# Optimization experiments

Hardware: AMD Instinct MI355X
Metric: run time of the kernel (lower is better)

## Reference

```python
import jax, jax.numpy as jnp
import numpy as np

B, S, D = 4, 2048, 1024
H, HD = 16, 64
DFF = 4096
EPS = 1e-6


def setup_inputs() -> dict:
    key = jax.random.key(0)
    ks = jax.random.split(key, 16)
    sc = 0.02
    def w(k, shape):
        return jax.random.normal(k, shape, dtype=jnp.float32) * sc
    return {
        'x': jax.random.normal(ks[0], (B, S, D), dtype=jnp.float32),
        'wq': w(ks[1], (D, D)), 'bq': jnp.zeros((D,), jnp.float32),
        'wk': w(ks[2], (D, D)), 'bk': jnp.zeros((D,), jnp.float32),
        'wv': w(ks[3], (D, D)), 'bv': jnp.zeros((D,), jnp.float32),
        'wo': w(ks[4], (D, D)), 'bo': jnp.zeros((D,), jnp.float32),
        'w1': w(ks[5], (D, DFF)), 'b1': jnp.zeros((DFF,), jnp.float32),
        'w2': w(ks[6], (DFF, D)), 'b2': jnp.zeros((D,), jnp.float32),
        'ln1_a': jnp.ones((D,), jnp.float32), 'ln1_b': jnp.zeros((D,), jnp.float32),
        'ln2_a': jnp.ones((D,), jnp.float32), 'ln2_b': jnp.zeros((D,), jnp.float32),
    }


def layernorm(x, alpha, bias):
    # Matches torch module: std is unbiased (ddof=1), divide by (std + eps)
    mean = jnp.mean(x, axis=-1, keepdims=True)
    var = jnp.sum((x - mean) ** 2, axis=-1, keepdims=True) / (x.shape[-1] - 1)
    std = jnp.sqrt(var)
    return alpha * ((x - mean) / (std + EPS)) + bias


def mha(x, wq, bq, wk, bk, wv, bv, wo, bo):
    q = (x @ wq + bq).reshape(B, S, H, HD)
    k = (x @ wk + bk).reshape(B, S, H, HD)
    v = (x @ wv + bv).reshape(B, S, H, HD)
    scores = jnp.einsum('bqhd,bkhd->bhqk', q, k) / jnp.sqrt(jnp.float32(HD))
    attn = jax.nn.softmax(scores, axis=-1)
    out = jnp.einsum('bhqk,bkhd->bqhd', attn, v).reshape(B, S, D)
    return out @ wo + bo


def reference(x, wq, bq, wk, bk, wv, bv, wo, bo, w1, b1, w2, b2,
              ln1_a, ln1_b, ln2_a, ln2_b):
    # Residual 1: x + MHA(LN(x))   (dropout = identity, eval mode)
    x = x + mha(layernorm(x, ln1_a, ln1_b), wq, bq, wk, bk, wv, bv, wo, bo)
    # Residual 2: x + FFN(LN(x))
    h = layernorm(x, ln2_a, ln2_b)
    ffn = jax.nn.relu(h @ w1 + b1) @ w2 + b2
    return x + ffn
```

## Files before the change

### kernel.cpp

```cpp
#include <hip/hip_runtime.h>

#define S_ 2048
#define D_ 1024

typedef unsigned short u16;
typedef unsigned int u32;
typedef __bf16 bf16x8 __attribute__((ext_vector_type(8)));
typedef unsigned short us8 __attribute__((ext_vector_type(8)));
typedef unsigned short us4 __attribute__((ext_vector_type(4)));
typedef unsigned int u32x4 __attribute__((ext_vector_type(4)));
typedef float f32x4 __attribute__((ext_vector_type(4)));

#if __has_builtin(__builtin_amdgcn_exp2f)
#define EXP2(x) __builtin_amdgcn_exp2f(x)
#else
#define EXP2(x) exp2f(x)
#endif

static __device__ __forceinline__ u16 f2bf(float f) {
  unsigned u = __builtin_bit_cast(unsigned, f);
  u += 0x7fffu + ((u >> 16) & 1u);
  return (u16)(u >> 16);
}

static __device__ __forceinline__ unsigned cvtpk_bf16(float lo, float hi) {
  unsigned r;
  asm("v_cvt_pk_bf16_f32 %0, %1, %2" : "=v"(r) : "v"(lo), "v"(hi));
  return r;
}

static __device__ __forceinline__ f32x4 mfma16(bf16x8 a, bf16x8 b, f32x4 c) {
  return __builtin_amdgcn_mfma_f32_16x16x32_bf16(a, b, c, 0, 0, 0);
}

static __device__ __forceinline__ void gload16(const void* g, void* lds) {
  __builtin_amdgcn_global_load_lds((const __attribute__((address_space(1))) void*)g,
                                   (__attribute__((address_space(3))) void*)lds, 16, 0, 0);
}

__global__ __launch_bounds__(256) void prep_kernel(
    const float* __restrict__ wq, const float* __restrict__ wk, const float* __restrict__ wv,
    const float* __restrict__ wo, const float* __restrict__ w1, const float* __restrict__ w2,
    const float* __restrict__ bq, const float* __restrict__ bk, const float* __restrict__ bv,
    u16* __restrict__ wqkv, u16* __restrict__ wot, u16* __restrict__ w1t,
    u16* __restrict__ w2t, float* __restrict__ bcat, float qs) {
  const int bid = blockIdx.x;
  const int tx = threadIdx.x, ty = threadIdx.y;
  if (bid >= 12288) {
    const int i = (bid - 12288) * 256 + ty * 32 + tx;
    bcat[i] = (i < 1024) ? bq[i] * qs : ((i < 2048) ? bk[i - 1024] : bv[i - 2048]);
    return;
  }
  const float* in;
  u16* out;
  int K, N, idx;
  float sc = 1.0f;
  if (bid < 4096) {
    K = 1024; N = 1024; idx = bid & 1023;
    if (bid < 1024)      { in = wq; out = wqkv;             sc = qs; }
    else if (bid < 2048) { in = wk; out = wqkv + (1 << 20); }
    else if (bid < 3072) { in = wv; out = wqkv + (2 << 20); }
    else                 { in = wo; out = wot; }
  } else if (bid < 8192) {
    in = w1; out = w1t; K = 1024; N = 4096; idx = bid - 4096;
  } else {
    in = w2; out = w2t; K = 4096; N = 1024; idx = bid - 8192;
  }
  const int nb = N >> 5;
  const int n0 = (idx % nb) * 32, k0 = (idx / nb) * 32;
  __shared__ float t[32][33];
#pragma unroll
  for (int i = 0; i < 4; i++)
    t[ty + 8 * i][tx] = in[(size_t)(k0 + ty + 8 * i) * N + n0 + tx];
  __syncthreads();
#pragma unroll
  for (int i = 0; i < 4; i++)
    out[(size_t)(n0 + ty + 8 * i) * K + k0 + tx] = f2bf(t[tx][ty + 8 * i] * sc);
}

__global__ __launch_bounds__(256) void ln_kernel(const float* __restrict__ in,
                                                 u16* __restrict__ out,
                                                 const float* __restrict__ alpha,
                                                 const float* __restrict__ beta) {
  const int row = blockIdx.x;
  const int tid = threadIdx.x;
  const float4 v = *(const float4*)(in + (size_t)row * D_ + tid * 4);
  float s = v.x + v.y + v.z + v.w;
  float ss = v.x * v.x + v.y * v.y + v.z * v.z + v.w * v.w;
#pragma unroll
  for (int off = 32; off >= 1; off >>= 1) {
    s += __shfl_xor(s, off);
    ss += __shfl_xor(ss, off);
  }
  __shared__ float red[8];
  const int w = tid >> 6, lane = tid & 63;
  if (lane == 0) { red[w] = s; red[4 + w] = ss; }
  __syncthreads();
  s = red[0] + red[1] + red[2] + red[3];
  ss = red[4] + red[5] + red[6] + red[7];
  const float mean = s * (1.0f / D_);
  const float var = (ss - s * mean) * (1.0f / (D_ - 1));
  const float inv = 1.0f / (sqrtf(var) + 1e-6f);
  const int j = tid * 4;
  const float4 av = *(const float4*)(alpha + j);
  const float4 bv = *(const float4*)(beta + j);
  us4 o;
  o[0] = f2bf((v.x - mean) * inv * av.x + bv.x);
  o[1] = f2bf((v.y - mean) * inv * av.y + bv.y);
  o[2] = f2bf((v.z - mean) * inv * av.z + bv.z);
  o[3] = f2bf((v.w - mean) * inv * av.w + bv.w);
  *(us4*)(out + (size_t)row * D_ + j) = o;
}

template <int OM, bool RELU, bool RESID>
__global__ __launch_bounds__(512, 2) void gemm_bt(const u16* __restrict__ A,
                                                  const u16* __restrict__ Bt,
                                                  const float* __restrict__ bias,
                                                  const float* __restrict__ resid,
                                                  void* __restrict__ outp,
                                                  void* __restrict__ out1,
                                                  void* __restrict__ out2, int N, int K) {
  __shared__ u16 lds[3 * 24576];
  const int tid = threadIdx.x;
  const int lane = tid & 63, w = tid >> 6;
  const int g = lane >> 4, r = lane & 15;
  const int wr = w >> 1, wc = w & 1;

  const int gx = gridDim.x;
  const int nwg = gx * gridDim.y;
  const int orig = blockIdx.y * gx + blockIdx.x;
  const int nid = (orig & 7) * (nwg >> 3) + (orig >> 3);
  const int bx = nid % gx, by = nid / gx;
  const size_t row0 = (size_t)by * 256;
  const int col0 = bx * 128;

  float bias4[4];
#pragma unroll
  for (int n = 0; n < 4; n++) bias4[n] = bias[col0 + wc * 64 + n * 16 + r];

  f32x4 acc[4][4];
#pragma unroll
  for (int m = 0; m < 4; m++)
#pragma unroll
    for (int n = 0; n < 4; n++) {
      f32x4 z = {bias4[n], bias4[n], bias4[n], bias4[n]};
      acc[m][n] = z;
    }

  const int lrow = w * 8 + (lane >> 3);
  const int scol = 8 * ((lane & 7) ^ (lane >> 3));
  const u16* gA = A + (row0 + lrow) * (size_t)K + scol;
  const u16* gB = Bt + ((size_t)col0 + lrow) * (size_t)K + scol;
  const int nt = K >> 6;
  const int sw = (r & 7) << 3;

  int bufi = 0;
#pragma unroll
  for (int t0 = 0; t0 < 2; t0++) {
    u16* dA = lds + t0 * 24576 + w * 512;
#pragma unroll
    for (int j = 0; j < 4; j++) gload16(gA + (size_t)(j * 64) * K + t0 * 64, dA + j * 4096);
#pragma unroll
    for (int j = 0; j < 2; j++)
      gload16(gB + (size_t)(j * 64) * K + t0 * 64, dA + 16384 + j * 4096);
  }

  for (int t = 0; t < nt; ++t) {
    if (t + 1 < nt)
      asm volatile("s_waitcnt vmcnt(6)" ::: "memory");
    else
      asm volatile("s_waitcnt vmcnt(0)" ::: "memory");
    __builtin_amdgcn_s_barrier();
    asm volatile("" ::: "memory");
    const bool st = (t + 2 < nt);
    const int bn = (bufi + 2 >= 3) ? bufi - 1 : bufi + 2;
    u16* dS = lds + bn * 24576 + w * 512;
    const size_t ko = (size_t)(t + 2) * 64;
    const u16* As_ = lds + bufi * 24576;
    const u16* Bs_ = As_ + 16384;
    bf16x8 bfr[2][4];

#pragma unroll
    for (int p = 0; p < 4; ++p) {
      bf16x8 a0 = __builtin_bit_cast(
          bf16x8, *(const us8*)(As_ + (wr * 64 + p * 16 + r) * 64 + ((g * 8) ^ sw)));
      bf16x8 a1 = __builtin_bit_cast(
          bf16x8, *(const us8*)(As_ + (wr * 64 + p * 16 + r) * 64 + ((32 + g * 8) ^ sw)));
      if (p == 0) {
#pragma unroll
        for (int kk = 0; kk < 2; kk++)
#pragma unroll
          for (int n = 0; n < 4; n++)
            bfr[kk][n] = __builtin_bit_cast(
                bf16x8,
                *(const us8*)(Bs_ + (wc * 64 + n * 16 + r) * 64 + ((kk * 32 + g * 8) ^ sw)));
      }
      if (st) {
        if (p == 0) {
          gload16(gA + ko, dS);
          gload16(gA + (size_t)64 * K + ko, dS + 4096);
        } else if (p == 1) {
          gload16(gA + (size_t)128 * K + ko, dS + 8192);
          gload16(gA + (size_t)192 * K + ko, dS + 12288);
        } else if (p == 2) {
          gload16(gB + ko, dS + 16384);
          gload16(gB + (size_t)64 * K + ko, dS + 20480);
        }
      }
      asm volatile("s_waitcnt lgkmcnt(0)" ::: "memory");
      __builtin_amdgcn_sched_barrier(0);
      __builtin_amdgcn_s_setprio(1);
#pragma unroll
      for (int n = 0; n < 4; n++) {
        acc[p][n] = mfma16(a0, bfr[0][n], acc[p][n]);
        acc[p][n] = mfma16(a1, bfr[1][n], acc[p][n]);
      }
      __builtin_amdgcn_s_setprio(0);
      if (p < 3) __builtin_amdgcn_s_barrier();
    }
    bufi = (bufi == 2) ? 0 : bufi + 1;
  }

#pragma unroll
  for (int m = 0; m < 4; m++)
#pragma unroll
    for (int n = 0; n < 4; n++) {
      if (OM == 2) {
        const int seg = col0 >> 10;
        const int cl = (col0 & 1023) + wc * 64 + n * 16 + r;
        if (seg == 2) {
          const int head = cl >> 6, hd = cl & 63;
          const size_t rg0 = row0 + wr * 64 + m * 16 + 4 * g;
          const int b = (int)(rg0 >> 11), s0 = (int)(rg0 & 2047);
          const int s0p = (s0 & ~63) | (s0 & 32) | ((s0 << 1) & 24) | ((s0 >> 2) & 4);
          us4 o;
#pragma unroll
          for (int i = 0; i < 4; i++) o[i] = f2bf(acc[m][n][i]);
          *(us4*)((u16*)out2 + (((size_t)(b * 16 + head) * 64 + hd) * S_ + s0p)) = o;
        } else {
          u16* dst = (u16*)(seg == 0 ? outp : out1);
#pragma unroll
          for (int i = 0; i < 4; i++) {
            const size_t rg = row0 + wr * 64 + m * 16 + 4 * g + i;
            dst[rg * D_ + cl] = f2bf(acc[m][n][i]);
          }
        }
      } else {
#pragma unroll
        for (int i = 0; i < 4; i++) {
          const size_t rg = row0 + wr * 64 + m * 16 + 4 * g + i;
          const int cg = col0 + wc * 64 + n * 16 + r;
          float v = acc[m][n][i];
          if (RESID) v += resid[rg * N + cg];
          if (RELU) v = fmaxf(v, 0.0f);
          if (OM == 1)
            ((float*)outp)[rg * N + cg] = v;
          else
            ((u16*)outp)[rg * N + cg] = f2bf(v);
        }
      }
    }
}

template <bool RELU>
__global__ __launch_bounds__(512, 2) void gemm_bt256(const u16* __restrict__ A,
                                                     const u16* __restrict__ Bt,
                                                     const float* __restrict__ bias,
                                                     u16* __restrict__ outp, int N, int K) {
  __shared__ u16 lds[2 * 32768];
  const int tid = threadIdx.x;
  const int lane = tid & 63, w = tid >> 6;
  const int g = lane >> 4, r = lane & 15;
  const int wr = w >> 2, wc = w & 3;
  const int gx = gridDim.x;
  const int nwg = gx * gridDim.y;
  const int orig = blockIdx.y * gx + blockIdx.x;
  const int nid = (orig & 7) * (nwg >> 3) + (orig >> 3);
  const int bx = nid % gx, by = nid / gx;
  const size_t row0 = (size_t)by * 256;
  const int col0 = bx * 256;

  float bias4[4];
#pragma unroll
  for (int n = 0; n < 4; n++) bias4[n] = bias[col0 + wc * 64 + n * 16 + r];

  f32x4 acc[8][4];
#pragma unroll
  for (int m = 0; m < 8; m++)
#pragma unroll
    for (int n = 0; n < 4; n++) {
      f32x4 z = {bias4[n], bias4[n], bias4[n], bias4[n]};
      acc[m][n] = z;
    }

  const int lrow = tid >> 3;
  const int scol = 8 * ((tid & 7) ^ (lrow & 7));
  const u16* gA = A + (row0 + lrow) * (size_t)K + scol;
  const u16* gB = Bt + ((size_t)col0 + lrow) * (size_t)K + scol;
  const int nt = K >> 6;
  const int sw = (r & 7) << 3;

  {
    u16* d = lds + w * 512;
#pragma unroll
    for (int j = 0; j < 4; j++) gload16(gA + (size_t)(j * 64) * K, d + j * 4096);
#pragma unroll
    for (int j = 0; j < 4; j++) gload16(gB + (size_t)(j * 64) * K, d + 16384 + j * 4096);
  }

  for (int t = 0; t < nt; ++t) {
    const u16* As_ = lds + (t & 1) * 32768;
    const u16* Bs_ = As_ + 16384;
    if (t + 1 < nt) {
      u16* d = lds + ((t + 1) & 1) * 32768 + w * 512;
      const size_t ko = (size_t)(t + 1) * 64;
#pragma unroll
      for (int j = 0; j < 4; j++) gload16(gA + (size_t)(j * 64) * K + ko, d + j * 4096);
#pragma unroll
      for (int j = 0; j < 4; j++) gload16(gB + (size_t)(j * 64) * K + ko, d + 16384 + j * 4096);
      asm volatile("s_waitcnt vmcnt(8)" ::: "memory");
    } else {
      asm volatile("s_waitcnt vmcnt(0)" ::: "memory");
    }
    __builtin_amdgcn_s_barrier();
    asm volatile("" ::: "memory");

    bf16x8 bfr[2][4];
#pragma unroll
    for (int kk = 0; kk < 2; kk++)
#pragma unroll
      for (int n = 0; n < 4; n++)
        bfr[kk][n] = __builtin_bit_cast(
            bf16x8, *(const us8*)(Bs_ + (wc * 64 + n * 16 + r) * 64 + ((kk * 32 + g * 8) ^ sw)));

#pragma unroll
    for (int p = 0; p < 4; ++p) {
      bf16x8 af[2][2];
#pragma unroll
      for (int mm = 0; mm < 2; mm++) {
        const int row = wr * 128 + (p * 2 + mm) * 16 + r;
        af[0][mm] = __builtin_bit_cast(bf16x8, *(const us8*)(As_ + row * 64 + ((g * 8) ^ sw)));
        af[1][mm] =
            __builtin_bit_cast(bf16x8, *(const us8*)(As_ + row * 64 + ((32 + g * 8) ^ sw)));
      }
      asm volatile("" ::: "memory");
      if (p > 0) __builtin_amdgcn_s_barrier();
      asm volatile("s_waitcnt lgkmcnt(0)" ::: "memory");
      __builtin_amdgcn_sched_barrier(0);
      __builtin_amdgcn_s_setprio(1);
#pragma unroll
      for (int mm = 0; mm < 2; mm++)
#pragma unroll
        for (int n = 0; n < 4; n++) {
          acc[p * 2 + mm][n] = mfma16(af[0][mm], bfr[0][n], acc[p * 2 + mm][n]);
          acc[p * 2 + mm][n] = mfma16(af[1][mm], bfr[1][n], acc[p * 2 + mm][n]);
        }
      __builtin_amdgcn_s_setprio(0);
    }
    asm volatile("" ::: "memory");
    __builtin_amdgcn_s_barrier();
  }

#pragma unroll
  for (int m = 0; m < 8; m++)
#pragma unroll
    for (int n = 0; n < 4; n++)
#pragma unroll
      for (int i = 0; i < 4; i++) {
        const size_t rg = row0 + wr * 128 + m * 16 + 4 * g + i;
        const int cg = col0 + wc * 64 + n * 16 + r;
        float v = acc[m][n][i];
        if (RELU) v = fmaxf(v, 0.0f);
        outp[rg * N + cg] = f2bf(v);
      }
}

__global__ __launch_bounds__(256) void attn_kernel(const u16* __restrict__ Q,
                                                   const u16* __restrict__ Km,
                                                   const u16* __restrict__ Vt_g,
                                                   u16* __restrict__ O) {
  __shared__ u16 Klds[2 * 4096];
  __shared__ u16 Vlds[2 * 4096];
  const int tid = threadIdx.x;
  const int lane = tid & 63, w = tid >> 6;
  const int g = lane >> 4, r = lane & 15;
  const int bh = blockIdx.y;
  const int b = bh >> 4, head = bh & 15;
  const size_t rowbase = (size_t)b * S_;
  const int colbase = head * 64;
  const int qw = blockIdx.x * 128 + w * 32;

  bf16x8 qf0[2], qf1[2];
#pragma unroll
  for (int qh = 0; qh < 2; qh++) {
    const u16* qrow = Q + (rowbase + qw + qh * 16 + r) * D_ + colbase;
    qf0[qh] = __builtin_bit_cast(bf16x8, *(const us8*)(qrow + g * 8));
    qf1[qh] = __builtin_bit_cast(bf16x8, *(const us8*)(qrow + 32 + g * 8));
  }

  const int srow = tid >> 3;
  const int sslot = (tid & 7) ^ (srow & 7);
  const u16* Kg = Km + (rowbase + srow) * D_ + colbase + sslot * 8;
  const u16* Vg = Vt_g + ((size_t)bh * 64 + srow) * S_ + sslot * 8;
  char* lK = (char*)Klds + w * 1024;
  char* lV = (char*)Vlds + w * 1024;

  const us8 onesw = {0x3F80, 0x3F80, 0x3F80, 0x3F80, 0x3F80, 0x3F80, 0x3F80, 0x3F80};
  const bf16x8 ones8 = __builtin_bit_cast(bf16x8, onesw);

  f32x4 lacc[2];
  f32x4 oacc[2][4];
#pragma unroll
  for (int qh = 0; qh < 2; qh++) {
    f32x4 z = {0.0f, 0.0f, 0.0f, 0.0f};
    lacc[qh] = z;
#pragma unroll
    for (int n = 0; n < 4; n++) oacc[qh][n] = z;
  }

  constexpr int NT = S_ / 64;
  gload16(Kg, lK);
  gload16(Kg + (size_t)32 * D_, lK + 4096);
  gload16(Vg, lV);
  gload16(Vg + (size_t)32 * S_, lV + 4096);
  gload16(Kg + (size_t)64 * D_, lK + 8192);
  gload16(Kg + (size_t)96 * D_, lK + 8192 + 4096);
  asm volatile("s_waitcnt vmcnt(2)" ::: "memory");
  __builtin_amdgcn_s_barrier();
  asm volatile("" ::: "memory");

  bf16x8 pa0[2], pa1[2];

  for (int kt = 0; kt < NT; ++kt) {
    const u16* Kc = Klds + (kt & 1) * 4096;
    const u16* Vp = Vlds + ((kt - 1) & 1) * 4096;

    f32x4 st[4][2];
    __builtin_amdgcn_s_setprio(1);
#pragma unroll
    for (int f = 0; f < 4; f++) {
      const int row = f * 16 + r;
      const int sw7 = row & 7;
      const bf16x8 k0 = __builtin_bit_cast(bf16x8, *(const us8*)(Kc + row * 64 + (g ^ sw7) * 8));
      const bf16x8 k1 =
          __builtin_bit_cast(bf16x8, *(const us8*)(Kc + row * 64 + ((g + 4) ^ sw7) * 8));
#pragma unroll
      for (int qh = 0; qh < 2; qh++) {
        f32x4 z = {0.0f, 0.0f, 0.0f, 0.0f};
        st[f][qh] = mfma16(k0, qf0[qh], z);
        st[f][qh] = mfma16(k1, qf1[qh], st[f][qh]);
      }
    }
    __builtin_amdgcn_s_setprio(0);

    if (kt > 0) {
      __builtin_amdgcn_s_setprio(1);
#pragma unroll
      for (int qh = 0; qh < 2; qh++) {
        lacc[qh] = mfma16(pa0[qh], ones8, lacc[qh]);
        lacc[qh] = mfma16(pa1[qh], ones8, lacc[qh]);
      }
#pragma unroll
      for (int n = 0; n < 4; n++) {
        const int row = n * 16 + r;
        const int sw7 = r & 7;
        const bf16x8 vb0 =
            __builtin_bit_cast(bf16x8, *(const us8*)(Vp + row * 64 + (g ^ sw7) * 8));
        const bf16x8 vb1 =
            __builtin_bit_cast(bf16x8, *(const us8*)(Vp + row * 64 + ((4 + g) ^ sw7) * 8));
#pragma unroll
        for (int qh = 0; qh < 2; qh++) {
          oacc[qh][n] = mfma16(pa0[qh], vb0, oacc[qh][n]);
          oacc[qh][n] = mfma16(pa1[qh], vb1, oacc[qh][n]);
        }
      }
      __builtin_amdgcn_s_setprio(0);
    }

    u32 pw[2][8];
#pragma unroll
    for (int qh = 0; qh < 2; qh++)
#pragma unroll
      for (int f = 0; f < 4; f++) {
        const float e0 = EXP2(st[f][qh][0]);
        const float e1 = EXP2(st[f][qh][1]);
        const float e2 = EXP2(st[f][qh][2]);
        const float e3 = EXP2(st[f][qh][3]);
        pw[qh][f * 2] = cvtpk_bf16(e0, e1);
        pw[qh][f * 2 + 1] = cvtpk_bf16(e2, e3);
      }
#pragma unroll
    for (int qh = 0; qh < 2; qh++) {
      const u32x4 a0w = {pw[qh][0], pw[qh][1], pw[qh][2], pw[qh][3]};
      const u32x4 a1w = {pw[qh][4], pw[qh][5], pw[qh][6], pw[qh][7]};
      pa0[qh] = __builtin_bit_cast(bf16x8, a0w);
      pa1[qh] = __builtin_bit_cast(bf16x8, a1w);
    }

    __builtin_amdgcn_s_barrier();
    asm volatile("" ::: "memory");

    if (kt + 2 < NT) {
      gload16(Kg + (size_t)(kt + 2) * 64 * D_, (char*)Klds + (kt & 1) * 8192 + w * 1024);
      gload16(Kg + (size_t)((kt + 2) * 64 + 32) * D_,
              (char*)Klds + (kt & 1) * 8192 + w * 1024 + 4096);
    }
    if (kt + 1 < NT) {
      gload16(Vg + (size_t)(kt + 1) * 64, (char*)Vlds + ((kt + 1) & 1) * 8192 + w * 1024);
      gload16(Vg + (size_t)32 * S_ + (size_t)(kt + 1) * 64,
              (char*)Vlds + ((kt + 1) & 1) * 8192 + w * 1024 + 4096);
    }
    if (kt + 2 < NT)
      asm volatile("s_waitcnt vmcnt(4)" ::: "memory");
    else if (kt + 1 < NT)
      asm volatile("s_waitcnt vmcnt(2)" ::: "memory");
    else
      asm volatile("s_waitcnt vmcnt(0)" ::: "memory");
    __builtin_amdgcn_s_barrier();
    asm volatile("" ::: "memory");
  }

  {
    const u16* Vp = Vlds + ((NT - 1) & 1) * 4096;
#pragma unroll
    for (int qh = 0; qh < 2; qh++) {
      lacc[qh] = mfma16(pa0[qh], ones8, lacc[qh]);
      lacc[qh] = mfma16(pa1[qh], ones8, lacc[qh]);
    }
#pragma unroll
    for (int n = 0; n < 4; n++) {
      const int row = n * 16 + r;
      const int sw7 = r & 7;
      const bf16x8 vb0 = __builtin_bit_cast(bf16x8, *(const us8*)(Vp + row * 64 + (g ^ sw7) * 8));
      const bf16x8 vb1 =
          __builtin_bit_cast(bf16x8, *(const us8*)(Vp + row * 64 + ((4 + g) ^ sw7) * 8));
#pragma unroll
      for (int qh = 0; qh < 2; qh++) {
        oacc[qh][n] = mfma16(pa0[qh], vb0, oacc[qh][n]);
        oacc[qh][n] = mfma16(pa1[qh], vb1, oacc[qh][n]);
      }
    }
  }

#pragma unroll
  for (int qh = 0; qh < 2; qh++) {
    float ld[4];
#pragma unroll
    for (int i = 0; i < 4; i++) ld[i] = 1.0f / lacc[qh][i];
#pragma unroll
    for (int n = 0; n < 4; n++)
#pragma unroll
      for (int i = 0; i < 4; i++)
        O[(rowbase + qw + qh * 16 + 4 * g + i) * D_ + colbase + n * 16 + r] =
            f2bf(oacc[qh][n][i] * ld[i]);
  }
}

extern "C" void kernel_launch(void* const* d_in, const int* in_sizes, int n_in, void* d_out,
                              int out_size, void* d_ws, size_t ws_size, hipStream_t stream) {
  (void)in_sizes; (void)n_in; (void)out_size; (void)ws_size;
  const float* x = (const float*)d_in[0];
  const float* wq = (const float*)d_in[1];
  const float* bq = (const float*)d_in[2];
  const float* wk = (const float*)d_in[3];
  const float* bk = (const float*)d_in[4];
  const float* wv = (const float*)d_in[5];
  const float* bv = (const float*)d_in[6];
  const float* wo = (const float*)d_in[7];
  const float* bo = (const float*)d_in[8];
  const float* w1 = (const float*)d_in[9];
  const float* b1 = (const float*)d_in[10];
  const float* w2 = (const float*)d_in[11];
  const float* b2 = (const float*)d_in[12];
  const float* ln1a = (const float*)d_in[13];
  const float* ln1b = (const float*)d_in[14];
  const float* ln2a = (const float*)d_in[15];
  const float* ln2b = (const float*)d_in[16];

  char* ws = (char*)d_ws;
  const size_t MB = 1ull << 20;
  u16* wqkv = (u16*)(ws + 0 * MB);
  u16* wot = (u16*)(ws + 6 * MB);
  u16* w1t = (u16*)(ws + 8 * MB);
  u16* w2t = (u16*)(ws + 16 * MB);
  u16* xA = (u16*)(ws + 24 * MB);
  u16* qb = (u16*)(ws + 40 * MB);
  u16* kb = (u16*)(ws + 56 * MB);
  u16* vt = (u16*)(ws + 72 * MB);
  float* bcat = (float*)(ws + 88 * MB);
  u16* ff1 = (u16*)(ws + 40 * MB);
  float* x1 = (float*)(ws + 104 * MB);

  const float QSCALE = 0.125f * 1.4426950408889634f;

  prep_kernel<<<12300, dim3(32, 8), 0, stream>>>(wq, wk, wv, wo, w1, w2, bq, bk, bv, wqkv, wot,
                                                 w1t, w2t, bcat, QSCALE);

  ln_kernel<<<8192, 256, 0, stream>>>(x, xA, ln1a, ln1b);
  gemm_bt<2, false, false><<<dim3(24, 32), 512, 0, stream>>>(xA, wqkv, bcat, nullptr, qb, kb, vt,
                                                             3072, 1024);
  attn_kernel<<<dim3(16, 64), 256, 0, stream>>>(qb, kb, vt, xA);
  gemm_bt<1, false, true><<<dim3(8, 32), 512, 0, stream>>>(xA, wot, bo, x, x1, nullptr, nullptr,
                                                           1024, 1024);
  ln_kernel<<<8192, 256, 0, stream>>>(x1, xA, ln2a, ln2b);
  gemm_bt256<true><<<dim3(16, 32), 512, 0, stream>>>(xA, w1t, b1, ff1, 4096, 1024);
  gemm_bt<1, false, true><<<dim3(8, 32), 512, 0, stream>>>(ff1, w2t, b2, x1, (float*)d_out,
                                                           nullptr, nullptr, 1024, 4096);
}
```

Measured before the change: 366.3 us.

## Shrink GEMM tiles to 128x128 with double buffering and remap attention blocks

Replaces the 256x128-tile, 8-wave, triple-buffered GEMM with a 128x128-tile, 4-wave, double-buffered variant. It is used for the QKV, output-projection and FFN2 GEMMs, doubling the grid. B fragments are loaded once per k-step and the next tile's loads are issued at the top of each iteration. The attention kernel gets an XCD-aware block remap so blocks of the same head share a die. The intent is better CU occupancy and wave balance on the smaller-N GEMMs and better L2 locality, at the cost of less data reuse per tile and shallower prefetch.

```diff
diff --git a/kernel.cpp b/kernel.cpp
--- a/kernel.cpp
+++ b/kernel.cpp
@@ -112,26 +112,25 @@
   *(us4*)(out + (size_t)row * D_ + j) = o;
 }
 
-template <int OM, bool RELU, bool RESID>
-__global__ __launch_bounds__(512, 2) void gemm_bt(const u16* __restrict__ A,
-                                                  const u16* __restrict__ Bt,
-                                                  const float* __restrict__ bias,
-                                                  const float* __restrict__ resid,
-                                                  void* __restrict__ outp,
-                                                  void* __restrict__ out1,
-                                                  void* __restrict__ out2, int N, int K) {
-  __shared__ u16 lds[3 * 24576];
+template <int OM, bool RESID>
+__global__ __launch_bounds__(256, 2) void gemm_bt128(const u16* __restrict__ A,
+                                                     const u16* __restrict__ Bt,
+                                                     const float* __restrict__ bias,
+                                                     const float* __restrict__ resid,
+                                                     void* __restrict__ outp,
+                                                     void* __restrict__ out1,
+                                                     void* __restrict__ out2, int N, int K) {
+  __shared__ u16 lds[2 * 16384];
   const int tid = threadIdx.x;
   const int lane = tid & 63, w = tid >> 6;
   const int g = lane >> 4, r = lane & 15;
   const int wr = w >> 1, wc = w & 1;
-
   const int gx = gridDim.x;
   const int nwg = gx * gridDim.y;
   const int orig = blockIdx.y * gx + blockIdx.x;
   const int nid = (orig & 7) * (nwg >> 3) + (orig >> 3);
   const int bx = nid % gx, by = nid / gx;
-  const size_t row0 = (size_t)by * 256;
+  const size_t row0 = (size_t)by * 128;
   const int col0 = bx * 128;
 
   float bias4[4];
@@ -147,66 +146,53 @@
       acc[m][n] = z;
     }
 
-  const int lrow = w * 8 + (lane >> 3);
-  const int scol = 8 * ((lane & 7) ^ (lane >> 3));
+  const int lrow = tid >> 3;
+  const int scol = 8 * ((tid & 7) ^ (lrow & 7));
   const u16* gA = A + (row0 + lrow) * (size_t)K + scol;
   const u16* gB = Bt + ((size_t)col0 + lrow) * (size_t)K + scol;
   const int nt = K >> 6;
   const int sw = (r & 7) << 3;
 
-  int bufi = 0;
-#pragma unroll
-  for (int t0 = 0; t0 < 2; t0++) {
-    u16* dA = lds + t0 * 24576 + w * 512;
-#pragma unroll
-    for (int j = 0; j < 4; j++) gload16(gA + (size_t)(j * 64) * K + t0 * 64, dA + j * 4096);
-#pragma unroll
-    for (int j = 0; j < 2; j++)
-      gload16(gB + (size_t)(j * 64) * K + t0 * 64, dA + 16384 + j * 4096);
+  {
+    u16* d = lds + w * 512;
+#pragma unroll
+    for (int j = 0; j < 4; j++) gload16(gA + (size_t)(j * 32) * K, d + j * 2048);
+#pragma unroll
+    for (int j = 0; j < 4; j++) gload16(gB + (size_t)(j * 32) * K, d + 8192 + j * 2048);
   }
 
   for (int t = 0; t < nt; ++t) {
-    if (t + 1 < nt)
-      asm volatile("s_waitcnt vmcnt(6)" ::: "memory");
-    else
+    const u16* As_ = lds + (t & 1) * 16384;
+    const u16* Bs_ = As_ + 8192;
+    if (t + 1 < nt) {
+      u16* d = lds + ((t + 1) & 1) * 16384 + w * 512;
+      const size_t ko = (size_t)(t + 1) * 64;
+#pragma unroll
+      for (int j = 0; j < 4; j++) gload16(gA + (size_t)(j * 32) * K + ko, d + j * 2048);
+#pragma unroll
+      for (int j = 0; j < 4; j++) gload16(gB + (size_t)(j * 32) * K + ko, d + 8192 + j * 2048);
+      asm volatile("s_waitcnt vmcnt(8)" ::: "memory");
+    } else {
       asm volatile("s_waitcnt vmcnt(0)" ::: "memory");
+    }
     __builtin_amdgcn_s_barrier();
     asm volatile("" ::: "memory");
-    const bool st = (t + 2 < nt);
-    const int bn = (bufi + 2 >= 3) ? bufi - 1 : bufi + 2;
-    u16* dS = lds + bn * 24576 + w * 512;
-    const size_t ko = (size_t)(t + 2) * 64;
-    const u16* As_ = lds + bufi * 24576;
-    const u16* Bs_ = As_ + 16384;
+
     bf16x8 bfr[2][4];
+#pragma unroll
+    for (int kk = 0; kk < 2; kk++)
+#pragma unroll
+      for (int n = 0; n < 4; n++)
+        bfr[kk][n] = __builtin_bit_cast(
+            bf16x8, *(const us8*)(Bs_ + (wc * 64 + n * 16 + r) * 64 + ((kk * 32 + g * 8) ^ sw)));
 
 #pragma unroll
     for (int p = 0; p < 4; ++p) {
-      bf16x8 a0 = __builtin_bit_cast(
-          bf16x8, *(const us8*)(As_ + (wr * 64 + p * 16 + r) * 64 + ((g * 8) ^ sw)));
-      bf16x8 a1 = __builtin_bit_cast(
-          bf16x8, *(const us8*)(As_ + (wr * 64 + p * 16 + r) * 64 + ((32 + g * 8) ^ sw)));
-      if (p == 0) {
-#pragma unroll
-        for (int kk = 0; kk < 2; kk++)
-#pragma unroll
-          for (int n = 0; n < 4; n++)
-            bfr[kk][n] = __builtin_bit_cast(
-                bf16x8,
-                *(const us8*)(Bs_ + (wc * 64 + n * 16 + r) * 64 + ((kk * 32 + g * 8) ^ sw)));
-      }
-      if (st) {
-        if (p == 0) {
-          gload16(gA + ko, dS);
-          gload16(gA + (size_t)64 * K + ko, dS + 4096);
-        } else if (p == 1) {
-          gload16(gA + (size_t)128 * K + ko, dS + 8192);
-          gload16(gA + (size_t)192 * K + ko, dS + 12288);
-        } else if (p == 2) {
-          gload16(gB + ko, dS + 16384);
-          gload16(gB + (size_t)64 * K + ko, dS + 20480);
-        }
-      }
+      const int row = wr * 64 + p * 16 + r;
+      bf16x8 a0 = __builtin_bit_cast(bf16x8, *(const us8*)(As_ + row * 64 + ((g * 8) ^ sw)));
+      bf16x8 a1 = __builtin_bit_cast(bf16x8, *(const us8*)(As_ + row * 64 + ((32 + g * 8) ^ sw)));
+      asm volatile("" ::: "memory");
+      if (p > 0) __builtin_amdgcn_s_barrier();
       asm volatile("s_waitcnt lgkmcnt(0)" ::: "memory");
       __builtin_amdgcn_sched_barrier(0);
       __builtin_amdgcn_s_setprio(1);
@@ -216,9 +202,9 @@
         acc[p][n] = mfma16(a1, bfr[1][n], acc[p][n]);
       }
       __builtin_amdgcn_s_setprio(0);
-      if (p < 3) __builtin_amdgcn_s_barrier();
-    }
-    bufi = (bufi == 2) ? 0 : bufi + 1;
+    }
+    asm volatile("" ::: "memory");
+    __builtin_amdgcn_s_barrier();
   }
 
 #pragma unroll
@@ -252,11 +238,7 @@
           const int cg = col0 + wc * 64 + n * 16 + r;
           float v = acc[m][n][i];
           if (RESID) v += resid[rg * N + cg];
-          if (RELU) v = fmaxf(v, 0.0f);
-          if (OM == 1)
-            ((float*)outp)[rg * N + cg] = v;
-          else
-            ((u16*)outp)[rg * N + cg] = f2bf(v);
+          ((float*)outp)[rg * N + cg] = v;
         }
       }
     }
@@ -384,11 +366,13 @@
   const int tid = threadIdx.x;
   const int lane = tid & 63, w = tid >> 6;
   const int g = lane >> 4, r = lane & 15;
-  const int bh = blockIdx.y;
+  const int orig = blockIdx.y * 16 + blockIdx.x;
+  const int nid = (orig & 7) * 128 + (orig >> 3);
+  const int qblk = nid & 15, bh = nid >> 4;
   const int b = bh >> 4, head = bh & 15;
   const size_t rowbase = (size_t)b * S_;
   const int colbase = head * 64;
-  const int qw = blockIdx.x * 128 + w * 32;
+  const int qw = qblk * 128 + w * 32;
 
   bf16x8 qf0[2], qf1[2];
 #pragma unroll
@@ -597,13 +581,13 @@
                                                  w1t, w2t, bcat, QSCALE);
 
   ln_kernel<<<8192, 256, 0, stream>>>(x, xA, ln1a, ln1b);
-  gemm_bt<2, false, false><<<dim3(24, 32), 512, 0, stream>>>(xA, wqkv, bcat, nullptr, qb, kb, vt,
-                                                             3072, 1024);
+  gemm_bt128<2, false><<<dim3(24, 64), 256, 0, stream>>>(xA, wqkv, bcat, nullptr, qb, kb, vt,
+                                                         3072, 1024);
   attn_kernel<<<dim3(16, 64), 256, 0, stream>>>(qb, kb, vt, xA);
-  gemm_bt<1, false, true><<<dim3(8, 32), 512, 0, stream>>>(xA, wot, bo, x, x1, nullptr, nullptr,
-                                                           1024, 1024);
+  gemm_bt128<1, true><<<dim3(8, 64), 256, 0, stream>>>(xA, wot, bo, x, x1, nullptr, nullptr,
+                                                       1024, 1024);
   ln_kernel<<<8192, 256, 0, stream>>>(x1, xA, ln2a, ln2b);
   gemm_bt256<true><<<dim3(16, 32), 512, 0, stream>>>(xA, w1t, b1, ff1, 4096, 1024);
-  gemm_bt<1, false, true><<<dim3(8, 32), 512, 0, stream>>>(ff1, w2t, b2, x1, (float*)d_out,
-                                                           nullptr, nullptr, 1024, 4096);
-}
+  gemm_bt128<1, true><<<dim3(8, 64), 256, 0, stream>>>(ff1, w2t, b2, x1, (float*)d_out,
+                                                       nullptr, nullptr, 1024, 4096);
+}
```

Measured after the change: 346.8 us. -5.3%, faster.
